# Kernel optimization log

Measured on AMD Instinct MI355X. Metric: run time of the kernel, lower is better.

The kernel has to match this reference:

```python
import jax, jax.numpy as jnp
import numpy as np

N = 100000   # nodes
E = 1600000  # edges
S = 4        # state_dimension
H = 64       # hidden_channels


def _gcn_conv(x, row, col, W, b):
    """PyG GCNConv: h = x @ W; add self-loops; symmetric deg^-1/2 norm; scatter-add; + bias."""
    n = x.shape[0]
    h = x @ W  # [N, out]
    loop = jnp.arange(n, dtype=row.dtype)
    r = jnp.concatenate([row, loop])  # sources (with self-loops)
    c = jnp.concatenate([col, loop])  # targets (with self-loops)
    deg = jax.ops.segment_sum(jnp.ones(r.shape[0], h.dtype), c, num_segments=n)
    dinv = jnp.where(deg > 0, jax.lax.rsqrt(deg), 0.0)
    norm = dinv[r] * dinv[c]                      # [E+N]
    msg = h[r] * norm[:, None]                    # gather + scale, [E+N, out]
    out = jax.ops.segment_sum(msg, c, num_segments=n)  # scatter-add
    return out + b


def setup_inputs() -> dict:
    key = jax.random.key(0)
    k1, k2, k3, k4 = jax.random.split(key, 4)
    x = jax.random.normal(k1, (N, S), dtype=jnp.float32)
    edge_index = jax.random.randint(k2, (2, E), 0, N, dtype=jnp.int32)
    # Glorot-ish init for the two GCNConv linear layers (+ zero bias, PyG default)
    W1 = jax.random.normal(k3, (S, H), dtype=jnp.float32) * (1.0 / np.sqrt(S))
    b1 = jnp.zeros((H,), jnp.float32)
    W2 = jax.random.normal(k4, (H, S), dtype=jnp.float32) * (1.0 / np.sqrt(H))
    b2 = jnp.zeros((S,), jnp.float32)
    return {"x": x, "edge_index": edge_index, "W1": W1, "b1": b1, "W2": W2, "b2": b2}


def reference(x, edge_index, W1, b1, W2, b2):
    row, col = edge_index[0], edge_index[1]
    h = _gcn_conv(x, row, col, W1, b1)
    h = jax.nn.relu(h)
    out = _gcn_conv(h, row, col, W2, b2)
    return out
```

## Files before the change

### kernel.cpp

```cpp
#include <hip/hip_runtime.h>


#define CSHIFT  9
#define CNODES  512
#define EPB     8192
#define PTH     1024
#define SEGC    96
#define CAPB    9216
#define ANODES  128
#define ACAP    2432

__global__ void __launch_bounds__(PTH) k_part(
        const int* __restrict__ row, const int* __restrict__ col,
        int e, int Kc, int* __restrict__ gcur, unsigned* __restrict__ dense) {
    __shared__ unsigned st[196 * SEGC];
    __shared__ int cur[196];
    __shared__ int gb[196];
    int t = threadIdx.x, bx = blockIdx.x;
    if (t < 196) cur[t] = 0;
    __syncthreads();
    int lo = bx * EPB;
    int cbuf[8], rbuf[8];
#pragma unroll
    for (int k = 0; k < 8; ++k) {
        int i = lo + t + k * PTH;
        if (i < e) { cbuf[k] = col[i]; rbuf[k] = row[i]; }
        else { cbuf[k] = -1; rbuf[k] = 0; }
    }
#pragma unroll
    for (int k = 0; k < 8; ++k) {
        int c = cbuf[k];
        if (c < 0) continue;
        int b = c >> CSHIFT;
        int j = atomicAdd(&cur[b], 1);
        if (j < SEGC)
            st[b * SEGC + j] = ((unsigned)rbuf[k] << CSHIFT)
                             | (unsigned)(c & (CNODES - 1));
    }
    __syncthreads();
    if (t < Kc) gb[t] = atomicAdd(&gcur[t], min(cur[t], SEGC));
    __syncthreads();
    int wv = t >> 6, lane = t & 63;
    for (int b = wv; b < Kc; b += 16) {
        int wb = min(cur[b], SEGC);
        int g0 = gb[b];
        for (int j = lane; j < wb; j += 64) {
            int pos = g0 + j;
            if (pos < CAPB) dense[(size_t)b * CAPB + pos] = st[b * SEGC + j];
        }
    }
}

__global__ void __launch_bounds__(1024) k_sort(
        const int* __restrict__ gcur, const unsigned* __restrict__ dense,
        unsigned* __restrict__ sortedg, int* __restrict__ rstart,
        const float4* __restrict__ x, float* __restrict__ dinv,
        float4* __restrict__ y, int n) {
    __shared__ int hist[CNODES];
    __shared__ int cur[CNODES];
    __shared__ unsigned sorted[CAPB];
    __shared__ int wsum[8], wpre[8];
    int b = blockIdx.x, t = threadIdx.x, lane = t & 63, wv = t >> 6;
    if (t < CNODES) hist[t] = 0;
    __syncthreads();
    int m = min(gcur[b], CAPB);
    const unsigned* dr = dense + (size_t)b * CAPB;
    const uint4* dr4 = (const uint4*)dr;
    int m4 = m >> 2;
    for (int i = t; i < m4; i += 1024) {
        uint4 w = dr4[i];
        atomicAdd(&hist[w.x & (CNODES - 1)], 1);
        atomicAdd(&hist[w.y & (CNODES - 1)], 1);
        atomicAdd(&hist[w.z & (CNODES - 1)], 1);
        atomicAdd(&hist[w.w & (CNODES - 1)], 1);
    }
    for (int i = (m4 << 2) + t; i < m; i += 1024)
        atomicAdd(&hist[dr[i] & (CNODES - 1)], 1);
    __syncthreads();
    int hv = 0, v = 0;
    if (t < CNODES) {
        hv = hist[t];
        v = hv;
#pragma unroll
        for (int off = 1; off < 64; off <<= 1) {
            int u = __shfl_up(v, off);
            if (lane >= off) v += u;
        }
        if (lane == 63) wsum[wv] = v;
    }
    __syncthreads();
    if (t < 8) {
        int s = 0;
        for (int i = 0; i < t; ++i) s += wsum[i];
        wpre[t] = s;
    }
    __syncthreads();
    if (t < CNODES) {
        int pex = v + wpre[wv] - hv;
        cur[t] = pex;
        int node = (b << CSHIFT) + t;
        rstart[node] = b * CAPB + pex;
        if (node < n) {
            float di = rsqrtf((float)hv + 1.0f);
            dinv[node] = di;
            float4 xv = x[node];
            y[node] = make_float4(xv.x * di, xv.y * di, xv.z * di, xv.w * di);
        }
    }
    __syncthreads();
    for (int i = t; i < m; i += 1024) {
        unsigned rec = dr[i];
        int p = atomicAdd(&cur[rec & (CNODES - 1)], 1);
        if (p < CAPB) sorted[p] = rec >> CSHIFT;
    }
    __syncthreads();
    size_t d0 = (size_t)b * CAPB;
    for (int i = t; i < m; i += 1024) sortedg[d0 + i] = sorted[i];
}

__global__ void __launch_bounds__(512) k_mid(
        const unsigned* __restrict__ ere, const int* __restrict__ rstart,
        const int* __restrict__ gcur, const float* __restrict__ dinv,
        const float4* __restrict__ x, const float4* __restrict__ y,
        const float* __restrict__ W1, const float* __restrict__ b1,
        const float* __restrict__ W2, const float* __restrict__ b2,
        float4* __restrict__ z, float4* __restrict__ out, int n) {
    __shared__ unsigned recs[ACAP];
    __shared__ float sW1[256];
    __shared__ float sW2[320];
    __shared__ float sb1[64];
    __shared__ float sb2[4];
    int g = blockIdx.x, t = threadIdx.x;
    int nlo = g * ANODES;
    int b = nlo >> CSHIFT;
    int s0 = rstart[nlo];
    int e0 = ((g & 3) == 3) ? b * CAPB + min(gcur[b], CAPB)
                            : rstart[nlo + ANODES];
    int len = min(e0 - s0, ACAP);
    for (int i = t; i < len; i += 512) recs[i] = ere[s0 + i];
    if (t < 256) {
        sW1[t] = W1[t];
        sW2[(t >> 2) * 5 + (t & 3)] = W2[t];
    } else if (t < 320) sb1[t - 256] = b1[t - 256];
    else if (t < 324) sb2[t - 320] = b2[t - 320];
    __syncthreads();
    int tt = t >> 2, q = t & 3;
    int s = rstart[nlo + tt] - s0;
    int epos = (tt == ANODES - 1) ? len : min(rstart[nlo + tt + 1] - s0, len);
    float vx = 0.f, vy = 0.f, vz = 0.f, vw = 0.f;
    int i = s + q;
    while (i + 12 < epos) {
        int r0 = recs[i], r1 = recs[i + 4], r2 = recs[i + 8], r3 = recs[i + 12];
        float4 a0 = y[r0], a1 = y[r1], a2 = y[r2], a3 = y[r3];
        vx += a0.x + a1.x + a2.x + a3.x;
        vy += a0.y + a1.y + a2.y + a3.y;
        vz += a0.z + a1.z + a2.z + a3.z;
        vw += a0.w + a1.w + a2.w + a3.w;
        i += 16;
    }
    for (; i < epos; i += 4) {
        float4 a = y[recs[i]];
        vx += a.x; vy += a.y; vz += a.z; vw += a.w;
    }
    vx += __shfl_xor(vx, 1); vx += __shfl_xor(vx, 2);
    vy += __shfl_xor(vy, 1); vy += __shfl_xor(vy, 2);
    vz += __shfl_xor(vz, 1); vz += __shfl_xor(vz, 2);
    vw += __shfl_xor(vw, 1); vw += __shfl_xor(vw, 2);
    int node = nlo + tt;
    if (node < n) {
        float di = dinv[node], sl = di * di;
        float4 xv = x[node];
        float a0 = di * vx + xv.x * sl;
        float a1 = di * vy + xv.y * sl;
        float a2 = di * vz + xv.z * sl;
        float a3 = di * vw + xv.w * sl;
        float t0 = 0.f, t1 = 0.f, t2 = 0.f, t3 = 0.f;
        int j0 = q << 4;
#pragma unroll
        for (int k = 0; k < 16; ++k) {
            int j = j0 + k;
            float hh = sb1[j] + a0 * sW1[j] + a1 * sW1[64 + j]
                     + a2 * sW1[128 + j] + a3 * sW1[192 + j];
            hh = fmaxf(hh, 0.f);
            t0 += hh * sW2[j * 5 + 0];
            t1 += hh * sW2[j * 5 + 1];
            t2 += hh * sW2[j * 5 + 2];
            t3 += hh * sW2[j * 5 + 3];
        }
        t0 += __shfl_xor(t0, 1); t0 += __shfl_xor(t0, 2);
        t1 += __shfl_xor(t1, 1); t1 += __shfl_xor(t1, 2);
        t2 += __shfl_xor(t2, 1); t2 += __shfl_xor(t2, 2);
        t3 += __shfl_xor(t3, 1); t3 += __shfl_xor(t3, 2);
        if (q == 0) {
            z[node] = make_float4(t0 * di, t1 * di, t2 * di, t3 * di);
            out[node] = make_float4(sb2[0] + t0 * sl, sb2[1] + t1 * sl,
                                    sb2[2] + t2 * sl, sb2[3] + t3 * sl);
        }
    }
}

__global__ void __launch_bounds__(512) k_acc2(
        const unsigned* __restrict__ ere, const int* __restrict__ rstart,
        const int* __restrict__ gcur, const float* __restrict__ dinv,
        const float4* __restrict__ z, float4* __restrict__ out, int n) {
    __shared__ unsigned recs[ACAP];
    int g = blockIdx.x, t = threadIdx.x;
    int nlo = g * ANODES;
    int b = nlo >> CSHIFT;
    int s0 = rstart[nlo];
    int e0 = ((g & 3) == 3) ? b * CAPB + min(gcur[b], CAPB)
                            : rstart[nlo + ANODES];
    int len = min(e0 - s0, ACAP);
    for (int i = t; i < len; i += 512) recs[i] = ere[s0 + i];
    __syncthreads();
    int tt = t >> 2, q = t & 3;
    int s = rstart[nlo + tt] - s0;
    int epos = (tt == ANODES - 1) ? len : min(rstart[nlo + tt + 1] - s0, len);
    float vx = 0.f, vy = 0.f, vz = 0.f, vw = 0.f;
    int i = s + q;
    while (i + 12 < epos) {
        int r0 = recs[i], r1 = recs[i + 4], r2 = recs[i + 8], r3 = recs[i + 12];
        float4 a0 = z[r0], a1 = z[r1], a2 = z[r2], a3 = z[r3];
        vx += a0.x + a1.x + a2.x + a3.x;
        vy += a0.y + a1.y + a2.y + a3.y;
        vz += a0.z + a1.z + a2.z + a3.z;
        vw += a0.w + a1.w + a2.w + a3.w;
        i += 16;
    }
    for (; i < epos; i += 4) {
        float4 a = z[recs[i]];
        vx += a.x; vy += a.y; vz += a.z; vw += a.w;
    }
    vx += __shfl_xor(vx, 1); vx += __shfl_xor(vx, 2);
    vy += __shfl_xor(vy, 1); vy += __shfl_xor(vy, 2);
    vz += __shfl_xor(vz, 1); vz += __shfl_xor(vz, 2);
    vw += __shfl_xor(vw, 1); vw += __shfl_xor(vw, 2);
    int node = nlo + tt;
    if (q == 0 && node < n) {
        float di = dinv[node];
        float4 o = out[node];
        out[node] = make_float4(o.x + di * vx, o.y + di * vy,
                                o.z + di * vz, o.w + di * vw);
    }
}

extern "C" void kernel_launch(void* const* d_in, const int* in_sizes, int n_in,
                              void* d_out, int out_size, void* d_ws, size_t ws_size,
                              hipStream_t stream) {
    const float* x  = (const float*)d_in[0];
    const int* edge = (const int*)d_in[1];
    const float* W1 = (const float*)d_in[2];
    const float* b1 = (const float*)d_in[3];
    const float* W2 = (const float*)d_in[4];
    const float* b2 = (const float*)d_in[5];
    float* out = (float*)d_out;

    const int n = in_sizes[0] / 4;
    const int e = in_sizes[1] / 2;
    const int* row = edge;
    const int* col = edge + e;
    const int Kc = (n + CNODES - 1) >> CSHIFT;
    const int NB = (e + EPB - 1) / EPB;

    char* ws = (char*)d_ws;
    float* y    = (float*)ws;  ws += (size_t)4 * n * 4;
    float* zmid = (float*)ws;  ws += (size_t)4 * n * 4;
    float* dinv = (float*)ws;  ws += (size_t)n * 4;
    unsigned* dense = (unsigned*)ws;   ws += (size_t)Kc * CAPB * 4;
    unsigned* sortedg = (unsigned*)ws; ws += (size_t)Kc * CAPB * 4;
    int* rstart = (int*)ws;    ws += (size_t)Kc * CNODES * 4;
    int* gcur   = (int*)ws;    ws += (size_t)Kc * 4;

    const int ga = (n + ANODES - 1) / ANODES;

    hipMemsetAsync(gcur, 0, (size_t)Kc * 4, stream);
    k_part<<<NB, PTH, 0, stream>>>(row, col, e, Kc, gcur, dense);
    k_sort<<<Kc, 1024, 0, stream>>>(gcur, dense, sortedg, rstart,
                                    (const float4*)x, dinv, (float4*)y, n);
    k_mid<<<ga, 512, 0, stream>>>(sortedg, rstart, gcur, dinv, (const float4*)x,
                                  (const float4*)y, W1, b1, W2, b2,
                                  (float4*)zmid, (float4*)out, n);
    k_acc2<<<ga, 512, 0, stream>>>(sortedg, rstart, gcur, dinv,
                                   (const float4*)zmid, (float4*)out, n);
}
```

Baseline: 118.4 us.

## Fuse sort, layer-1 and layer-2 aggregation into one persistent kernel with grid barriers

Replaces the sort, mid and second-aggregation kernels with one persistent kernel of two blocks per 512-node bucket. Each block sorts its half-bucket's edges into shared memory and keeps them there for both aggregation phases, with software grid barriers between phases. This removes the global sortedg, rstart and dinv round-trips and two kernel launches. In exchange it relies on all 392 blocks of 1024 threads being co-resident for the spin barrier, and each bucket's dense records are now scanned twice, once per half.

```diff
diff --git a/kernel.cpp b/kernel.cpp
--- a/kernel.cpp
+++ b/kernel.cpp
@@ -3,12 +3,12 @@
 
 #define CSHIFT  9
 #define CNODES  512
+#define NHALF   256
 #define EPB     8192
 #define PTH     1024
 #define SEGC    96
 #define CAPB    9216
-#define ANODES  128
-#define ACAP    2432
+#define HCAP    4608
 
 __global__ void __launch_bounds__(PTH) k_part(
         const int* __restrict__ row, const int* __restrict__ col,
@@ -51,17 +51,58 @@
     }
 }
 
-__global__ void __launch_bounds__(1024) k_sort(
+__device__ __forceinline__ void gridbar(int* bar, int nblk) {
+    __syncthreads();
+    if (threadIdx.x == 0) {
+        __threadfence();
+        int g = __hip_atomic_load(&bar[1], __ATOMIC_RELAXED,
+                                  __HIP_MEMORY_SCOPE_AGENT);
+        if (atomicAdd(&bar[0], 1) == nblk - 1) {
+            __hip_atomic_store(&bar[0], 0, __ATOMIC_RELAXED,
+                               __HIP_MEMORY_SCOPE_AGENT);
+            __hip_atomic_store(&bar[1], g + 1, __ATOMIC_RELEASE,
+                               __HIP_MEMORY_SCOPE_AGENT);
+        } else {
+            while (__hip_atomic_load(&bar[1], __ATOMIC_ACQUIRE,
+                                     __HIP_MEMORY_SCOPE_AGENT) == g)
+                __builtin_amdgcn_s_sleep(2);
+        }
+        __threadfence();
+    }
+    __syncthreads();
+}
+
+struct Sm {
+    int hist[NHALF];
+    int cur[NHALF];
+    int rs[NHALF + 1];
+    float sdi[NHALF];
+    unsigned sorted[HCAP];
+    float sW1[256];
+    float sW2[320];
+    float sb1[64];
+    float sb2[4];
+    int wsum[4], wpre[4];
+};
+
+__global__ void __launch_bounds__(1024, 8) k_fused(
         const int* __restrict__ gcur, const unsigned* __restrict__ dense,
-        unsigned* __restrict__ sortedg, int* __restrict__ rstart,
-        const float4* __restrict__ x, float* __restrict__ dinv,
-        float4* __restrict__ y, int n) {
-    __shared__ int hist[CNODES];
-    __shared__ int cur[CNODES];
-    __shared__ unsigned sorted[CAPB];
-    __shared__ int wsum[8], wpre[8];
-    int b = blockIdx.x, t = threadIdx.x, lane = t & 63, wv = t >> 6;
-    if (t < CNODES) hist[t] = 0;
+        int* bar, int nblk,
+        const float4* __restrict__ x, float4* __restrict__ y,
+        const float* __restrict__ W1, const float* __restrict__ b1,
+        const float* __restrict__ W2, const float* __restrict__ b2,
+        float4* __restrict__ z, float4* __restrict__ out, int n) {
+    __shared__ Sm sm;
+    int bh = blockIdx.x, t = threadIdx.x;
+    int lane = t & 63, wv = t >> 6;
+    int b = bh >> 1, h = bh & 1;
+
+    if (t < 256) {
+        sm.sW1[t] = W1[t];
+        sm.sW2[(t >> 2) * 5 + (t & 3)] = W2[t];
+        sm.hist[t] = 0;
+    } else if (t < 320) sm.sb1[t - 256] = b1[t - 256];
+    else if (t < 324) sm.sb2[t - 320] = b2[t - 320];
     __syncthreads();
     int m = min(gcur[b], CAPB);
     const unsigned* dr = dense + (size_t)b * CAPB;
@@ -69,178 +110,152 @@
     int m4 = m >> 2;
     for (int i = t; i < m4; i += 1024) {
         uint4 w = dr4[i];
-        atomicAdd(&hist[w.x & (CNODES - 1)], 1);
-        atomicAdd(&hist[w.y & (CNODES - 1)], 1);
-        atomicAdd(&hist[w.z & (CNODES - 1)], 1);
-        atomicAdd(&hist[w.w & (CNODES - 1)], 1);
-    }
-    for (int i = (m4 << 2) + t; i < m; i += 1024)
-        atomicAdd(&hist[dr[i] & (CNODES - 1)], 1);
+        int l;
+        l = w.x & (CNODES - 1); if ((l >> 8) == h) atomicAdd(&sm.hist[l & 255], 1);
+        l = w.y & (CNODES - 1); if ((l >> 8) == h) atomicAdd(&sm.hist[l & 255], 1);
+        l = w.z & (CNODES - 1); if ((l >> 8) == h) atomicAdd(&sm.hist[l & 255], 1);
+        l = w.w & (CNODES - 1); if ((l >> 8) == h) atomicAdd(&sm.hist[l & 255], 1);
+    }
+    for (int i = (m4 << 2) + t; i < m; i += 1024) {
+        int l = dr[i] & (CNODES - 1);
+        if ((l >> 8) == h) atomicAdd(&sm.hist[l & 255], 1);
+    }
     __syncthreads();
     int hv = 0, v = 0;
-    if (t < CNODES) {
-        hv = hist[t];
+    if (t < NHALF) {
+        hv = sm.hist[t];
         v = hv;
 #pragma unroll
         for (int off = 1; off < 64; off <<= 1) {
             int u = __shfl_up(v, off);
             if (lane >= off) v += u;
         }
-        if (lane == 63) wsum[wv] = v;
-    }
-    __syncthreads();
-    if (t < 8) {
+        if (lane == 63) sm.wsum[wv] = v;
+    }
+    __syncthreads();
+    if (t < 4) {
         int s = 0;
-        for (int i = 0; i < t; ++i) s += wsum[i];
-        wpre[t] = s;
-    }
-    __syncthreads();
-    if (t < CNODES) {
-        int pex = v + wpre[wv] - hv;
-        cur[t] = pex;
-        int node = (b << CSHIFT) + t;
-        rstart[node] = b * CAPB + pex;
+        for (int i = 0; i < t; ++i) s += sm.wsum[i];
+        sm.wpre[t] = s;
+    }
+    __syncthreads();
+    if (t < NHALF) {
+        int incl = v + sm.wpre[wv];
+        int pex = incl - hv;
+        sm.cur[t] = pex;
+        sm.rs[t] = pex;
+        if (t == NHALF - 1) sm.rs[NHALF] = incl;
+        float di = rsqrtf((float)hv + 1.0f);
+        sm.sdi[t] = di;
+        int node = (b << CSHIFT) + (h << 8) + t;
         if (node < n) {
-            float di = rsqrtf((float)hv + 1.0f);
-            dinv[node] = di;
             float4 xv = x[node];
             y[node] = make_float4(xv.x * di, xv.y * di, xv.z * di, xv.w * di);
         }
     }
     __syncthreads();
-    for (int i = t; i < m; i += 1024) {
+    for (int i = t; i < m4; i += 1024) {
+        uint4 w = dr4[i];
+        int l = w.x & (CNODES - 1);
+        if ((l >> 8) == h) { int p = atomicAdd(&sm.cur[l & 255], 1); if (p < HCAP) sm.sorted[p] = w.x >> CSHIFT; }
+        l = w.y & (CNODES - 1);
+        if ((l >> 8) == h) { int p = atomicAdd(&sm.cur[l & 255], 1); if (p < HCAP) sm.sorted[p] = w.y >> CSHIFT; }
+        l = w.z & (CNODES - 1);
+        if ((l >> 8) == h) { int p = atomicAdd(&sm.cur[l & 255], 1); if (p < HCAP) sm.sorted[p] = w.z >> CSHIFT; }
+        l = w.w & (CNODES - 1);
+        if ((l >> 8) == h) { int p = atomicAdd(&sm.cur[l & 255], 1); if (p < HCAP) sm.sorted[p] = w.w >> CSHIFT; }
+    }
+    for (int i = (m4 << 2) + t; i < m; i += 1024) {
         unsigned rec = dr[i];
-        int p = atomicAdd(&cur[rec & (CNODES - 1)], 1);
-        if (p < CAPB) sorted[p] = rec >> CSHIFT;
-    }
-    __syncthreads();
-    size_t d0 = (size_t)b * CAPB;
-    for (int i = t; i < m; i += 1024) sortedg[d0 + i] = sorted[i];
-}
-
-__global__ void __launch_bounds__(512) k_mid(
-        const unsigned* __restrict__ ere, const int* __restrict__ rstart,
-        const int* __restrict__ gcur, const float* __restrict__ dinv,
-        const float4* __restrict__ x, const float4* __restrict__ y,
-        const float* __restrict__ W1, const float* __restrict__ b1,
-        const float* __restrict__ W2, const float* __restrict__ b2,
-        float4* __restrict__ z, float4* __restrict__ out, int n) {
-    __shared__ unsigned recs[ACAP];
-    __shared__ float sW1[256];
-    __shared__ float sW2[320];
-    __shared__ float sb1[64];
-    __shared__ float sb2[4];
-    int g = blockIdx.x, t = threadIdx.x;
-    int nlo = g * ANODES;
-    int b = nlo >> CSHIFT;
-    int s0 = rstart[nlo];
-    int e0 = ((g & 3) == 3) ? b * CAPB + min(gcur[b], CAPB)
-                            : rstart[nlo + ANODES];
-    int len = min(e0 - s0, ACAP);
-    for (int i = t; i < len; i += 512) recs[i] = ere[s0 + i];
-    if (t < 256) {
-        sW1[t] = W1[t];
-        sW2[(t >> 2) * 5 + (t & 3)] = W2[t];
-    } else if (t < 320) sb1[t - 256] = b1[t - 256];
-    else if (t < 324) sb2[t - 320] = b2[t - 320];
-    __syncthreads();
+        int l = rec & (CNODES - 1);
+        if ((l >> 8) == h) { int p = atomicAdd(&sm.cur[l & 255], 1); if (p < HCAP) sm.sorted[p] = rec >> CSHIFT; }
+    }
+    gridbar(bar, nblk);
+
     int tt = t >> 2, q = t & 3;
-    int s = rstart[nlo + tt] - s0;
-    int epos = (tt == ANODES - 1) ? len : min(rstart[nlo + tt + 1] - s0, len);
-    float vx = 0.f, vy = 0.f, vz = 0.f, vw = 0.f;
-    int i = s + q;
-    while (i + 12 < epos) {
-        int r0 = recs[i], r1 = recs[i + 4], r2 = recs[i + 8], r3 = recs[i + 12];
-        float4 a0 = y[r0], a1 = y[r1], a2 = y[r2], a3 = y[r3];
-        vx += a0.x + a1.x + a2.x + a3.x;
-        vy += a0.y + a1.y + a2.y + a3.y;
-        vz += a0.z + a1.z + a2.z + a3.z;
-        vw += a0.w + a1.w + a2.w + a3.w;
-        i += 16;
-    }
-    for (; i < epos; i += 4) {
-        float4 a = y[recs[i]];
-        vx += a.x; vy += a.y; vz += a.z; vw += a.w;
-    }
-    vx += __shfl_xor(vx, 1); vx += __shfl_xor(vx, 2);
-    vy += __shfl_xor(vy, 1); vy += __shfl_xor(vy, 2);
-    vz += __shfl_xor(vz, 1); vz += __shfl_xor(vz, 2);
-    vw += __shfl_xor(vw, 1); vw += __shfl_xor(vw, 2);
-    int node = nlo + tt;
-    if (node < n) {
-        float di = dinv[node], sl = di * di;
-        float4 xv = x[node];
-        float a0 = di * vx + xv.x * sl;
-        float a1 = di * vy + xv.y * sl;
-        float a2 = di * vz + xv.z * sl;
-        float a3 = di * vw + xv.w * sl;
-        float t0 = 0.f, t1 = 0.f, t2 = 0.f, t3 = 0.f;
-        int j0 = q << 4;
-#pragma unroll
-        for (int k = 0; k < 16; ++k) {
-            int j = j0 + k;
-            float hh = sb1[j] + a0 * sW1[j] + a1 * sW1[64 + j]
-                     + a2 * sW1[128 + j] + a3 * sW1[192 + j];
-            hh = fmaxf(hh, 0.f);
-            t0 += hh * sW2[j * 5 + 0];
-            t1 += hh * sW2[j * 5 + 1];
-            t2 += hh * sW2[j * 5 + 2];
-            t3 += hh * sW2[j * 5 + 3];
-        }
-        t0 += __shfl_xor(t0, 1); t0 += __shfl_xor(t0, 2);
-        t1 += __shfl_xor(t1, 1); t1 += __shfl_xor(t1, 2);
-        t2 += __shfl_xor(t2, 1); t2 += __shfl_xor(t2, 2);
-        t3 += __shfl_xor(t3, 1); t3 += __shfl_xor(t3, 2);
-        if (q == 0) {
-            z[node] = make_float4(t0 * di, t1 * di, t2 * di, t3 * di);
-            out[node] = make_float4(sb2[0] + t0 * sl, sb2[1] + t1 * sl,
-                                    sb2[2] + t2 * sl, sb2[3] + t3 * sl);
-        }
-    }
-}
-
-__global__ void __launch_bounds__(512) k_acc2(
-        const unsigned* __restrict__ ere, const int* __restrict__ rstart,
-        const int* __restrict__ gcur, const float* __restrict__ dinv,
-        const float4* __restrict__ z, float4* __restrict__ out, int n) {
-    __shared__ unsigned recs[ACAP];
-    int g = blockIdx.x, t = threadIdx.x;
-    int nlo = g * ANODES;
-    int b = nlo >> CSHIFT;
-    int s0 = rstart[nlo];
-    int e0 = ((g & 3) == 3) ? b * CAPB + min(gcur[b], CAPB)
-                            : rstart[nlo + ANODES];
-    int len = min(e0 - s0, ACAP);
-    for (int i = t; i < len; i += 512) recs[i] = ere[s0 + i];
-    __syncthreads();
-    int tt = t >> 2, q = t & 3;
-    int s = rstart[nlo + tt] - s0;
-    int epos = (tt == ANODES - 1) ? len : min(rstart[nlo + tt + 1] - s0, len);
-    float vx = 0.f, vy = 0.f, vz = 0.f, vw = 0.f;
-    int i = s + q;
-    while (i + 12 < epos) {
-        int r0 = recs[i], r1 = recs[i + 4], r2 = recs[i + 8], r3 = recs[i + 12];
-        float4 a0 = z[r0], a1 = z[r1], a2 = z[r2], a3 = z[r3];
-        vx += a0.x + a1.x + a2.x + a3.x;
-        vy += a0.y + a1.y + a2.y + a3.y;
-        vz += a0.z + a1.z + a2.z + a3.z;
-        vw += a0.w + a1.w + a2.w + a3.w;
-        i += 16;
-    }
-    for (; i < epos; i += 4) {
-        float4 a = z[recs[i]];
-        vx += a.x; vy += a.y; vz += a.z; vw += a.w;
-    }
-    vx += __shfl_xor(vx, 1); vx += __shfl_xor(vx, 2);
-    vy += __shfl_xor(vy, 1); vy += __shfl_xor(vy, 2);
-    vz += __shfl_xor(vz, 1); vz += __shfl_xor(vz, 2);
-    vw += __shfl_xor(vw, 1); vw += __shfl_xor(vw, 2);
-    int node = nlo + tt;
-    if (q == 0 && node < n) {
-        float di = dinv[node];
-        float4 o = out[node];
-        out[node] = make_float4(o.x + di * vx, o.y + di * vy,
-                                o.z + di * vz, o.w + di * vw);
+    int s = min(sm.rs[tt], HCAP);
+    int epos = min(sm.rs[tt + 1], HCAP);
+    int node = (b << CSHIFT) + (h << 8) + tt;
+    float di = sm.sdi[tt], sl = di * di;
+    {
+        float vx = 0.f, vy = 0.f, vz = 0.f, vw = 0.f;
+        int i = s + q;
+        while (i + 12 < epos) {
+            int r0 = sm.sorted[i], r1 = sm.sorted[i + 4];
+            int r2 = sm.sorted[i + 8], r3 = sm.sorted[i + 12];
+            float4 a0 = y[r0], a1 = y[r1], a2 = y[r2], a3 = y[r3];
+            vx += a0.x + a1.x + a2.x + a3.x;
+            vy += a0.y + a1.y + a2.y + a3.y;
+            vz += a0.z + a1.z + a2.z + a3.z;
+            vw += a0.w + a1.w + a2.w + a3.w;
+            i += 16;
+        }
+        for (; i < epos; i += 4) {
+            float4 a = y[sm.sorted[i]];
+            vx += a.x; vy += a.y; vz += a.z; vw += a.w;
+        }
+        vx += __shfl_xor(vx, 1); vx += __shfl_xor(vx, 2);
+        vy += __shfl_xor(vy, 1); vy += __shfl_xor(vy, 2);
+        vz += __shfl_xor(vz, 1); vz += __shfl_xor(vz, 2);
+        vw += __shfl_xor(vw, 1); vw += __shfl_xor(vw, 2);
+        if (node < n) {
+            float4 xv = x[node];
+            float a0 = di * vx + xv.x * sl;
+            float a1 = di * vy + xv.y * sl;
+            float a2 = di * vz + xv.z * sl;
+            float a3 = di * vw + xv.w * sl;
+            float t0 = 0.f, t1 = 0.f, t2 = 0.f, t3 = 0.f;
+            int j0 = q << 4;
+#pragma unroll
+            for (int k = 0; k < 16; ++k) {
+                int j = j0 + k;
+                float hh = sm.sb1[j] + a0 * sm.sW1[j] + a1 * sm.sW1[64 + j]
+                         + a2 * sm.sW1[128 + j] + a3 * sm.sW1[192 + j];
+                hh = fmaxf(hh, 0.f);
+                t0 += hh * sm.sW2[j * 5 + 0];
+                t1 += hh * sm.sW2[j * 5 + 1];
+                t2 += hh * sm.sW2[j * 5 + 2];
+                t3 += hh * sm.sW2[j * 5 + 3];
+            }
+            t0 += __shfl_xor(t0, 1); t0 += __shfl_xor(t0, 2);
+            t1 += __shfl_xor(t1, 1); t1 += __shfl_xor(t1, 2);
+            t2 += __shfl_xor(t2, 1); t2 += __shfl_xor(t2, 2);
+            t3 += __shfl_xor(t3, 1); t3 += __shfl_xor(t3, 2);
+            if (q == 0) {
+                z[node] = make_float4(t0 * di, t1 * di, t2 * di, t3 * di);
+                out[node] = make_float4(sm.sb2[0] + t0 * sl, sm.sb2[1] + t1 * sl,
+                                        sm.sb2[2] + t2 * sl, sm.sb2[3] + t3 * sl);
+            }
+        }
+    }
+    gridbar(bar, nblk);
+
+    {
+        float vx = 0.f, vy = 0.f, vz = 0.f, vw = 0.f;
+        int i = s + q;
+        while (i + 12 < epos) {
+            int r0 = sm.sorted[i], r1 = sm.sorted[i + 4];
+            int r2 = sm.sorted[i + 8], r3 = sm.sorted[i + 12];
+            float4 a0 = z[r0], a1 = z[r1], a2 = z[r2], a3 = z[r3];
+            vx += a0.x + a1.x + a2.x + a3.x;
+            vy += a0.y + a1.y + a2.y + a3.y;
+            vz += a0.z + a1.z + a2.z + a3.z;
+            vw += a0.w + a1.w + a2.w + a3.w;
+            i += 16;
+        }
+        for (; i < epos; i += 4) {
+            float4 a = z[sm.sorted[i]];
+            vx += a.x; vy += a.y; vz += a.z; vw += a.w;
+        }
+        vx += __shfl_xor(vx, 1); vx += __shfl_xor(vx, 2);
+        vy += __shfl_xor(vy, 1); vy += __shfl_xor(vy, 2);
+        vz += __shfl_xor(vz, 1); vz += __shfl_xor(vz, 2);
+        vw += __shfl_xor(vw, 1); vw += __shfl_xor(vw, 2);
+        if (q == 0 && node < n) {
+            float4 o = out[node];
+            out[node] = make_float4(o.x + di * vx, o.y + di * vy,
+                                    o.z + di * vz, o.w + di * vw);
+        }
     }
 }
 
@@ -265,21 +280,16 @@
     char* ws = (char*)d_ws;
     float* y    = (float*)ws;  ws += (size_t)4 * n * 4;
     float* zmid = (float*)ws;  ws += (size_t)4 * n * 4;
-    float* dinv = (float*)ws;  ws += (size_t)n * 4;
     unsigned* dense = (unsigned*)ws;   ws += (size_t)Kc * CAPB * 4;
-    unsigned* sortedg = (unsigned*)ws; ws += (size_t)Kc * CAPB * 4;
-    int* rstart = (int*)ws;    ws += (size_t)Kc * CNODES * 4;
     int* gcur   = (int*)ws;    ws += (size_t)Kc * 4;
-
-    const int ga = (n + ANODES - 1) / ANODES;
-
-    hipMemsetAsync(gcur, 0, (size_t)Kc * 4, stream);
+    int* bar    = (int*)ws;    ws += 2 * 4;
+
+    const int nblk = 2 * Kc;
+
+    hipMemsetAsync(gcur, 0, (size_t)(Kc + 2) * 4, stream);
     k_part<<<NB, PTH, 0, stream>>>(row, col, e, Kc, gcur, dense);
-    k_sort<<<Kc, 1024, 0, stream>>>(gcur, dense, sortedg, rstart,
-                                    (const float4*)x, dinv, (float4*)y, n);
-    k_mid<<<ga, 512, 0, stream>>>(sortedg, rstart, gcur, dinv, (const float4*)x,
-                                  (const float4*)y, W1, b1, W2, b2,
-                                  (float4*)zmid, (float4*)out, n);
-    k_acc2<<<ga, 512, 0, stream>>>(sortedg, rstart, gcur, dinv,
-                                   (const float4*)zmid, (float4*)out, n);
-}
+    k_fused<<<nblk, 1024, 0, stream>>>(gcur, dense, bar, nblk,
+                                       (const float4*)x, (float4*)y,
+                                       W1, b1, W2, b2,
+                                       (float4*)zmid, (float4*)out, n);
+}
```

New measurement: 245.6 us. 2.07x slower.

## Split per-bucket sort into two half-bucket blocks and vectorize partition loads

Applied to the files above, without the earlier changes.

The counting-sort kernel now launches two blocks per destination bucket, and each block handles one half of the 512 local nodes. Both blocks read the whole bucket, but each keeps only its own records and writes to its own region. This doubles parallelism across CUs and halves the LDS each block needs. The partition kernel processes 4096 edges per block with int4 vectorized loads and a smaller per-bucket staging capacity (SEGC 64), which raises block count and occupancy. The costs are that each bucket's dense records are read twice, and the smaller staging segments raise the chance that capacity limits drop overflowing edges.

```diff
diff --git a/kernel.cpp b/kernel.cpp
--- a/kernel.cpp
+++ b/kernel.cpp
@@ -3,14 +3,15 @@
 
 #define CSHIFT  9
 #define CNODES  512
-#define EPB     8192
+#define EPB     4096
 #define PTH     1024
-#define SEGC    96
+#define SEGC    64
 #define CAPB    9216
+#define HCAP    4608
 #define ANODES  128
 #define ACAP    2432
 
-__global__ void __launch_bounds__(PTH) k_part(
+__global__ void __launch_bounds__(PTH, 8) k_part(
         const int* __restrict__ row, const int* __restrict__ col,
         int e, int Kc, int* __restrict__ gcur, unsigned* __restrict__ dense) {
     __shared__ unsigned st[196 * SEGC];
@@ -20,21 +21,29 @@
     if (t < 196) cur[t] = 0;
     __syncthreads();
     int lo = bx * EPB;
-    int cbuf[8], rbuf[8];
+    int cb[4], rb[4];
+    int i0 = lo + (t << 2);
+    if (i0 + 3 < e) {
+        int4 c4 = ((const int4*)col)[(lo >> 2) + t];
+        int4 r4 = ((const int4*)row)[(lo >> 2) + t];
+        cb[0] = c4.x; cb[1] = c4.y; cb[2] = c4.z; cb[3] = c4.w;
+        rb[0] = r4.x; rb[1] = r4.y; rb[2] = r4.z; rb[3] = r4.w;
+    } else {
 #pragma unroll
-    for (int k = 0; k < 8; ++k) {
-        int i = lo + t + k * PTH;
-        if (i < e) { cbuf[k] = col[i]; rbuf[k] = row[i]; }
-        else { cbuf[k] = -1; rbuf[k] = 0; }
+        for (int k = 0; k < 4; ++k) {
+            int i = i0 + k;
+            if (i < e) { cb[k] = col[i]; rb[k] = row[i]; }
+            else { cb[k] = -1; rb[k] = 0; }
+        }
     }
 #pragma unroll
-    for (int k = 0; k < 8; ++k) {
-        int c = cbuf[k];
+    for (int k = 0; k < 4; ++k) {
+        int c = cb[k];
         if (c < 0) continue;
         int b = c >> CSHIFT;
         int j = atomicAdd(&cur[b], 1);
         if (j < SEGC)
-            st[b * SEGC + j] = ((unsigned)rbuf[k] << CSHIFT)
+            st[b * SEGC + j] = ((unsigned)rb[k] << CSHIFT)
                              | (unsigned)(c & (CNODES - 1));
     }
     __syncthreads();
@@ -51,17 +60,18 @@
     }
 }
 
-__global__ void __launch_bounds__(1024) k_sort(
+__global__ void __launch_bounds__(1024, 8) k_sortH(
         const int* __restrict__ gcur, const unsigned* __restrict__ dense,
         unsigned* __restrict__ sortedg, int* __restrict__ rstart,
         const float4* __restrict__ x, float* __restrict__ dinv,
         float4* __restrict__ y, int n) {
-    __shared__ int hist[CNODES];
-    __shared__ int cur[CNODES];
-    __shared__ unsigned sorted[CAPB];
-    __shared__ int wsum[8], wpre[8];
-    int b = blockIdx.x, t = threadIdx.x, lane = t & 63, wv = t >> 6;
-    if (t < CNODES) hist[t] = 0;
+    __shared__ int hist[256];
+    __shared__ int cur[256];
+    __shared__ unsigned sorted[HCAP];
+    __shared__ int wsum[4], wpre[4];
+    int bh = blockIdx.x, b = bh >> 1, h = bh & 1;
+    int t = threadIdx.x, lane = t & 63, wv = t >> 6;
+    if (t < 256) hist[t] = 0;
     __syncthreads();
     int m = min(gcur[b], CAPB);
     const unsigned* dr = dense + (size_t)b * CAPB;
@@ -69,16 +79,19 @@
     int m4 = m >> 2;
     for (int i = t; i < m4; i += 1024) {
         uint4 w = dr4[i];
-        atomicAdd(&hist[w.x & (CNODES - 1)], 1);
-        atomicAdd(&hist[w.y & (CNODES - 1)], 1);
-        atomicAdd(&hist[w.z & (CNODES - 1)], 1);
-        atomicAdd(&hist[w.w & (CNODES - 1)], 1);
-    }
-    for (int i = (m4 << 2) + t; i < m; i += 1024)
-        atomicAdd(&hist[dr[i] & (CNODES - 1)], 1);
+        int l;
+        l = w.x & (CNODES - 1); if ((l >> 8) == h) atomicAdd(&hist[l & 255], 1);
+        l = w.y & (CNODES - 1); if ((l >> 8) == h) atomicAdd(&hist[l & 255], 1);
+        l = w.z & (CNODES - 1); if ((l >> 8) == h) atomicAdd(&hist[l & 255], 1);
+        l = w.w & (CNODES - 1); if ((l >> 8) == h) atomicAdd(&hist[l & 255], 1);
+    }
+    for (int i = (m4 << 2) + t; i < m; i += 1024) {
+        int l = dr[i] & (CNODES - 1);
+        if ((l >> 8) == h) atomicAdd(&hist[l & 255], 1);
+    }
     __syncthreads();
     int hv = 0, v = 0;
-    if (t < CNODES) {
+    if (t < 256) {
         hv = hist[t];
         v = hv;
 #pragma unroll
@@ -89,17 +102,19 @@
         if (lane == 63) wsum[wv] = v;
     }
     __syncthreads();
-    if (t < 8) {
+    if (t < 4) {
         int s = 0;
         for (int i = 0; i < t; ++i) s += wsum[i];
         wpre[t] = s;
     }
     __syncthreads();
-    if (t < CNODES) {
+    int cown = wsum[0] + wsum[1] + wsum[2] + wsum[3];
+    int base = h ? (m - cown) : 0;
+    if (t < 256) {
         int pex = v + wpre[wv] - hv;
         cur[t] = pex;
-        int node = (b << CSHIFT) + t;
-        rstart[node] = b * CAPB + pex;
+        int node = (b << CSHIFT) + (h << 8) + t;
+        rstart[node] = b * CAPB + base + pex;
         if (node < n) {
             float di = rsqrtf((float)hv + 1.0f);
             dinv[node] = di;
@@ -108,14 +123,26 @@
         }
     }
     __syncthreads();
-    for (int i = t; i < m; i += 1024) {
+    for (int i = t; i < m4; i += 1024) {
+        uint4 w = dr4[i];
+        int l = w.x & (CNODES - 1);
+        if ((l >> 8) == h) { int p = atomicAdd(&cur[l & 255], 1); if (p < HCAP) sorted[p] = w.x >> CSHIFT; }
+        l = w.y & (CNODES - 1);
+        if ((l >> 8) == h) { int p = atomicAdd(&cur[l & 255], 1); if (p < HCAP) sorted[p] = w.y >> CSHIFT; }
+        l = w.z & (CNODES - 1);
+        if ((l >> 8) == h) { int p = atomicAdd(&cur[l & 255], 1); if (p < HCAP) sorted[p] = w.z >> CSHIFT; }
+        l = w.w & (CNODES - 1);
+        if ((l >> 8) == h) { int p = atomicAdd(&cur[l & 255], 1); if (p < HCAP) sorted[p] = w.w >> CSHIFT; }
+    }
+    for (int i = (m4 << 2) + t; i < m; i += 1024) {
         unsigned rec = dr[i];
-        int p = atomicAdd(&cur[rec & (CNODES - 1)], 1);
-        if (p < CAPB) sorted[p] = rec >> CSHIFT;
-    }
-    __syncthreads();
-    size_t d0 = (size_t)b * CAPB;
-    for (int i = t; i < m; i += 1024) sortedg[d0 + i] = sorted[i];
+        int l = rec & (CNODES - 1);
+        if ((l >> 8) == h) { int p = atomicAdd(&cur[l & 255], 1); if (p < HCAP) sorted[p] = rec >> CSHIFT; }
+    }
+    __syncthreads();
+    int wb = min(cown, HCAP);
+    size_t d0 = (size_t)b * CAPB + base;
+    for (int i = t; i < wb; i += 1024) sortedg[d0 + i] = sorted[i];
 }
 
 __global__ void __launch_bounds__(512) k_mid(
@@ -275,8 +302,8 @@
 
     hipMemsetAsync(gcur, 0, (size_t)Kc * 4, stream);
     k_part<<<NB, PTH, 0, stream>>>(row, col, e, Kc, gcur, dense);
-    k_sort<<<Kc, 1024, 0, stream>>>(gcur, dense, sortedg, rstart,
-                                    (const float4*)x, dinv, (float4*)y, n);
+    k_sortH<<<2 * Kc, 1024, 0, stream>>>(gcur, dense, sortedg, rstart,
+                                         (const float4*)x, dinv, (float4*)y, n);
     k_mid<<<ga, 512, 0, stream>>>(sortedg, rstart, gcur, dinv, (const float4*)x,
                                   (const float4*)y, W1, b1, W2, b2,
                                   (float4*)zmid, (float4*)out, n);
```

Result: no change. 119.4 us (+0.8%).
